# Kernel tuning notes

Measured on AMD Instinct MI355X. Metric: run time of the kernel, lower is better.

## Reference

```python
import jax, jax.numpy as jnp
import numpy as np
from jax import lax

STRIDE = 8  # backbone patch-embed stride


def setup_inputs() -> dict:
    key = jax.random.key(0)
    ks = jax.random.split(key, 5)
    B, H, W = 2, 256, 256
    Cr, Cg, Cout = 256, 5, 256
    N = 65536  # memory bank size
    return {
        "image": jax.random.normal(ks[0], (B, 3, H, W), dtype=jnp.float32),
        "geometry_map": jax.random.uniform(ks[1], (B, Cg, H, W), dtype=jnp.float32),
        "backbone_w": jax.random.normal(ks[2], (Cr, 3, STRIDE, STRIDE), dtype=jnp.float32) * 0.05,
        "backbone_b": jnp.zeros((Cr,), dtype=jnp.float32),
        "fusion_w": jax.random.normal(ks[3], (Cout, Cr + Cg), dtype=jnp.float32) * 0.05,
        "fusion_b": jnp.zeros((Cout,), dtype=jnp.float32),
        "memory_bank": jax.random.normal(ks[4], (N, Cout), dtype=jnp.float32),
    }


def reference(image, geometry_map, backbone_w, backbone_b, fusion_w, fusion_b, memory_bank):
    # --- backbone: patch-embed conv + relu -> (B,Cr,H',W') ---
    feat_rgb = lax.conv_general_dilated(
        image, backbone_w, window_strides=(STRIDE, STRIDE), padding="VALID",
        dimension_numbers=("NCHW", "OIHW", "NCHW"))
    feat_rgb = jax.nn.relu(feat_rgb + backbone_b[None, :, None, None])
    B, Cr, H, W = feat_rgb.shape

    # --- bilinear align of geometry map (align_corners=False semantics) ---
    geo = jax.image.resize(geometry_map, (B, geometry_map.shape[1], H, W), method="bilinear")

    # --- fusion 1x1 conv ---
    fused = jnp.concatenate([feat_rgb, geo], axis=1)           # (B, Cr+Cg, H, W)
    fused = jnp.einsum("oc,bchw->bohw", fusion_w, fused) + fusion_b[None, :, None, None]
    C = fused.shape[1]

    # --- NN min-distance to memory bank (cdist + min) ---
    flat = fused.transpose(0, 2, 3, 1).reshape(-1, C)          # (M, C)
    d2 = (jnp.sum(flat * flat, axis=1)[:, None]
          + jnp.sum(memory_bank * memory_bank, axis=1)[None, :]
          - 2.0 * flat @ memory_bank.T)                        # (M, N)
    min_dist = jnp.sqrt(jnp.maximum(jnp.min(d2, axis=1), 0.0))  # sqrt monotone: min before sqrt
    score_plain = min_dist.reshape(B, H, W)

    # --- geometry reweighting (sigmoid mode, alpha=1.0) ---
    density, opacity, anis = geo[:, 3:4], geo[:, 2:3], geo[:, 4:5]
    base = 0.5 * density + 0.25 * (1.0 - opacity) + 0.25 * anis
    w = 1.0 + jax.nn.sigmoid(4.0 * (base - 0.5))               # (B,1,H,W)
    score_geo = score_plain * w[:, 0]
    return score_plain, score_geo
```

## Files before the change

kernel.cpp:

```cpp
#include <hip/hip_runtime.h>
#include <hip/hip_bf16.h>
#include <stdint.h>

typedef __attribute__((ext_vector_type(8))) short bf16x8;
typedef __attribute__((ext_vector_type(4))) float f32x4;

#define NP 2048
#define NBANK 65536
#define NCHUNKS 32
#define CHUNK 2048
#define SUBR 64
#define NSUB 32
#define CF 261

__device__ inline short f2bf(float f) {
  __hip_bfloat16 h = __float2bfloat16(f);
  return *reinterpret_cast<short*>(&h);
}

__global__ __launch_bounds__(256) void k_repack_fw(
    const float* __restrict__ fw, float* __restrict__ fwp)
{
  int idx = blockIdx.x * 256 + threadIdx.x;
  int o = idx / 264, c = idx % 264;
  fwp[idx] = (c < CF) ? fw[(size_t)o * CF + c] : 0.f;
}

__global__ __launch_bounds__(512) void k_prep(
    const float* __restrict__ image, const float* __restrict__ geometry,
    const float* __restrict__ bw, const float* __restrict__ bb,
    const float* __restrict__ fwp, const float* __restrict__ fb,
    const float* __restrict__ mb,
    short* __restrict__ flatb, float* __restrict__ qsq, float* __restrict__ wgt,
    short* __restrict__ mbb, float* __restrict__ msq)
{
  __shared__ float patch[1536];
  __shared__ float fusedS[8][264];
  __shared__ float gv[40][8];
  __shared__ float gw[40][8];
  __shared__ float redS[8][8];
  int t = threadIdx.x;
  int bid = blockIdx.x;

  if (bid >= 256) {
    int row = (bid - 256) * 8 + (t >> 6);
    int lane = t & 63;
    float4 v = ((const float4*)(mb + (size_t)row * 256))[lane];
    short4 o; o.x = f2bf(v.x); o.y = f2bf(v.y); o.z = f2bf(v.z); o.w = f2bf(v.w);
    ((short4*)(mbb + (size_t)row * 256))[lane] = o;
    float s = v.x*v.x + v.y*v.y + v.z*v.z + v.w*v.w;
    #pragma unroll
    for (int m = 1; m < 64; m <<= 1) s += __shfl_xor(s, m);
    if (lane == 0) msq[row] = s;
    return;
  }

  int b = bid >> 7, rem = bid & 127, h = rem >> 2, w0 = (rem & 3) * 8;

  #pragma unroll
  for (int j = 0; j < 3; j++) {
    int idx = t + j * 512;
    int c = idx >> 9, r = (idx >> 6) & 7, col = idx & 63;
    patch[idx] = image[(((size_t)(b*3 + c) * 256) + 8*h + r) * 256 + 8*w0 + col];
  }
  if (t >= 320 && t < 344) {
    int i = (t - 320) / 3, c = 261 + (t - 320) % 3;
    fusedS[i][c] = 0.f;
  }
  if (t < 320) {
    int v = t >> 3, sub = t & 7;
    int i = v / 5, cg = v % 5;
    int jj = w0 + i;
    float val = 0.f, ws = 0.f;
    const float* gch = geometry + (size_t)(b*5 + cg) * 65536;
    #pragma unroll
    for (int rr = 0; rr < 2; rr++) {
      int r = sub * 2 + rr;
      int gr = 8*h - 4 + r;
      float wr = 1.f - fabsf((float)r - 7.5f) * 0.125f;
      if (gr >= 0 && gr < 256) {
        const float* grow = gch + (size_t)gr * 256;
        for (int c = 0; c < 16; c++) {
          int gc = 8*jj - 4 + c;
          if (gc >= 0 && gc < 256) {
            float wc_ = 1.f - fabsf((float)c - 7.5f) * 0.125f;
            val += wr * wc_ * grow[gc];
            ws  += wr * wc_;
          }
        }
      }
    }
    gv[v][sub] = val; gw[v][sub] = ws;
  }
  __syncthreads();
  if (t < 40) {
    int i = t / 5, cg = t % 5;
    float sv = 0.f, sw = 0.f;
    #pragma unroll
    for (int u = 0; u < 8; u++) { sv += gv[t][u]; sw += gw[t][u]; }
    fusedS[i][256 + cg] = sv / sw;
  }

  int g = t >> 8, o = t & 255;
  float a4[4] = {0.f, 0.f, 0.f, 0.f};
  const float4* wo4 = (const float4*)(bw + (size_t)o * 192);
  for (int cr = 0; cr < 24; cr++) {
    const float* prow = &patch[cr * 64 + g * 32];
    #pragma unroll
    for (int half = 0; half < 2; half++) {
      float4 w4 = wo4[cr*2 + half];
      #pragma unroll
      for (int e = 0; e < 4; e++) {
        float wv = (&w4.x)[e];
        int cl = half*4 + e;
        #pragma unroll
        for (int i4 = 0; i4 < 4; i4++) a4[i4] += wv * prow[i4*8 + cl];
      }
    }
  }
  float bias = bb[o];
  #pragma unroll
  for (int i4 = 0; i4 < 4; i4++) fusedS[g*4 + i4][o] = fmaxf(a4[i4] + bias, 0.f);
  __syncthreads();

  #pragma unroll
  for (int i4 = 0; i4 < 4; i4++) a4[i4] = 0.f;
  const float4* fwo4 = (const float4*)(fwp + (size_t)o * 264);
  for (int c4 = 0; c4 < 66; c4++) {
    float4 w4 = fwo4[c4];
    #pragma unroll
    for (int e = 0; e < 4; e++) {
      float wv = (&w4.x)[e];
      int c = c4*4 + e;
      #pragma unroll
      for (int i4 = 0; i4 < 4; i4++) a4[i4] += wv * fusedS[g*4 + i4][c];
    }
  }
  float fbias = fb[o];
  int lane = t & 63, wid = t >> 6;
  #pragma unroll
  for (int i4 = 0; i4 < 4; i4++) {
    a4[i4] += fbias;
    int p = b*1024 + h*32 + w0 + g*4 + i4;
    flatb[(size_t)p * 256 + o] = f2bf(a4[i4]);
    float s = a4[i4] * a4[i4];
    #pragma unroll
    for (int m = 1; m < 64; m <<= 1) s += __shfl_xor(s, m);
    if (lane == 0) redS[g*4 + i4][wid & 3] = s;
  }
  __syncthreads();
  if (t < 8) {
    float s = redS[t][0] + redS[t][1] + redS[t][2] + redS[t][3];
    int p = b*1024 + h*32 + w0 + t;
    qsq[p] = s;
    float den = fusedS[t][256+3], opa = fusedS[t][256+2], ani = fusedS[t][256+4];
    float base2 = 0.5f*den + 0.25f*(1.f - opa) + 0.25f*ani;
    wgt[p] = 1.f + 1.f/(1.f + expf(-4.f*(base2 - 0.5f)));
  }
}

__global__ __launch_bounds__(256, 2) void k_distmin(
    const short* __restrict__ Aq, const short* __restrict__ Bb,
    const float* __restrict__ qsq, const float* __restrict__ msq,
    float* __restrict__ partial)
{
  __shared__ __align__(16) unsigned char sB[2][32768];
  __shared__ float msq_lds[2048];
  __shared__ float red[2][128];
  int t = threadIdx.x;
  int lane = t & 63, wid = t >> 6;
  int wr = wid >> 1, wc = wid & 1;
  const int l15 = lane & 15, l4 = lane >> 4;
  int nc = blockIdx.x, mt = blockIdx.y;
  int m0 = mt * 128;
  const size_t nchunk0 = (size_t)nc * CHUNK;
  const unsigned char* Bbyte = (const unsigned char*)Bb + nchunk0 * 512;
  const unsigned char* Abyte = (const unsigned char*)Aq;

  int soff[8];
  #pragma unroll
  for (int j = 0; j < 8; j++) {
    int sh = j * 4 + wid;
    int ks = sh & 7, hh = (sh >> 3) & 1, wcs = sh >> 4;
    int n = wcs * 32 + hh * 16 + l15;
    int k = ks * 64 + l4 * 16;
    soff[j] = n * 512 + k;
  }

  {
    const float4* src = (const float4*)(msq + nchunk0);
    float4* dst = (float4*)msq_lds;
    dst[t] = src[t];
    dst[t + 256] = src[t + 256];
  }

  bf16x8 af[4][8];
  #pragma unroll
  for (int mi = 0; mi < 4; mi++)
    #pragma unroll
    for (int ks = 0; ks < 8; ks++) {
      af[mi][ks] = *(const bf16x8*)(Abyte +
          (size_t)(m0 + wr*64 + mi*16 + l15) * 512 + ks*64 + l4*16);
      asm volatile("" : "+v"(af[mi][ks]));
    }

  float vmin[4][4];
  #pragma unroll
  for (int mi = 0; mi < 4; mi++)
    #pragma unroll
    for (int r = 0; r < 4; r++) vmin[mi][r] = 3.4e38f;

  __syncthreads();

#define STAGE(bufsel, sidx) do {                                              \
    const unsigned char* gb_ = Bbyte + (size_t)(sidx) * 32768;                \
    unsigned char* lb_ = &sB[bufsel][0] + wid * 1024;                         \
    _Pragma("unroll")                                                         \
    for (int j_ = 0; j_ < 8; j_++) {                                          \
      __builtin_amdgcn_global_load_lds(                                       \
        (const __attribute__((address_space(1))) unsigned int*)(gb_ + soff[j_]), \
        (__attribute__((address_space(3))) unsigned int*)(lb_ + j_*4096),     \
        16, 0, 0);                                                            \
    }                                                                         \
  } while (0)

#define ACQUIRE(N) do {                                                       \
    asm volatile("s_waitcnt vmcnt(" #N ")" ::: "memory");                     \
    __builtin_amdgcn_s_barrier();                                             \
    __builtin_amdgcn_sched_barrier(0);                                        \
  } while (0)

#define RELEASE() do {                                                        \
    asm volatile("s_waitcnt lgkmcnt(0)" ::: "memory");                        \
    __builtin_amdgcn_s_barrier();                                             \
    __builtin_amdgcn_sched_barrier(0);                                        \
  } while (0)

#define COMPUTE(sarg) do {                                                    \
    const unsigned char* buf_ = &sB[(sarg) & 1][0] + wc * 16384;              \
    float m0_ = msq_lds[(sarg) * 64 + wc * 32 + l15];                         \
    float m1_ = msq_lds[(sarg) * 64 + wc * 32 + 16 + l15];                    \
    f32x4 acc_[4][2];                                                         \
    _Pragma("unroll")                                                         \
    for (int mi = 0; mi < 4; mi++) {                                          \
      acc_[mi][0] = (f32x4){0.f,0.f,0.f,0.f};                                 \
      acc_[mi][1] = (f32x4){0.f,0.f,0.f,0.f};                                 \
    }                                                                         \
    __builtin_amdgcn_s_setprio(1);                                            \
    _Pragma("unroll")                                                         \
    for (int ks = 0; ks < 8; ks++) {                                          \
      bf16x8 b0_ = *(const bf16x8*)(buf_ + ks*1024 + l4*256 + l15*16);        \
      bf16x8 b1_ = *(const bf16x8*)(buf_ + 8192 + ks*1024 + l4*256 + l15*16); \
      _Pragma("unroll")                                                       \
      for (int mi = 0; mi < 4; mi++) {                                        \
        acc_[mi][0] = __builtin_amdgcn_mfma_f32_16x16x32_bf16(af[mi][ks], b0_, acc_[mi][0], 0, 0, 0); \
        acc_[mi][1] = __builtin_amdgcn_mfma_f32_16x16x32_bf16(af[mi][ks], b1_, acc_[mi][1], 0, 0, 0); \
      }                                                                       \
    }                                                                         \
    __builtin_amdgcn_s_setprio(0);                                            \
    _Pragma("unroll")                                                         \
    for (int mi = 0; mi < 4; mi++)                                            \
      _Pragma("unroll")                                                       \
      for (int r = 0; r < 4; r++)                                             \
        vmin[mi][r] = fminf(vmin[mi][r],                                      \
            fminf(m0_ - 2.f*acc_[mi][0][r], m1_ - 2.f*acc_[mi][1][r]));       \
  } while (0)

  STAGE(0, 0);
  STAGE(1, 1);

  for (int s = 0; s < NSUB - 2; s++) {
    ACQUIRE(8);
    COMPUTE(s);
    RELEASE();
    STAGE(s & 1, s + 2);
  }
  ACQUIRE(8);
  COMPUTE(NSUB - 2);
  ACQUIRE(0);
  COMPUTE(NSUB - 1);

#undef STAGE
#undef ACQUIRE
#undef RELEASE
#undef COMPUTE

  #pragma unroll
  for (int mi = 0; mi < 4; mi++)
    #pragma unroll
    for (int r = 0; r < 4; r++) {
      float v = vmin[mi][r];
      v = fminf(v, __shfl_xor(v, 1));
      v = fminf(v, __shfl_xor(v, 2));
      v = fminf(v, __shfl_xor(v, 4));
      v = fminf(v, __shfl_xor(v, 8));
      if (l15 == 0) red[wc][wr * 64 + mi * 16 + l4 * 4 + r] = v;
    }
  __syncthreads();
  if (t < 128) {
    float v = fminf(red[0][t], red[1][t]);
    float d2 = qsq[m0 + t] + v;
    partial[(size_t)(m0 + t) * NCHUNKS + nc] = fmaxf(d2, 0.f);
  }
}

__global__ __launch_bounds__(256) void k_final(
    const float* __restrict__ partial, const float* __restrict__ wgt,
    float* __restrict__ out)
{
  int q = blockIdx.x * 256 + threadIdx.x;
  const float4* p = (const float4*)(partial + (size_t)q * NCHUNKS);
  float v = 3.4e38f;
  #pragma unroll
  for (int j = 0; j < 8; j++) {
    float4 x = p[j];
    v = fminf(v, fminf(fminf(x.x, x.y), fminf(x.z, x.w)));
  }
  float sp = sqrtf(v);
  out[q] = sp;
  out[NP + q] = sp * wgt[q];
}

extern "C" void kernel_launch(void* const* d_in, const int* in_sizes, int n_in,
                              void* d_out, int out_size, void* d_ws, size_t ws_size,
                              hipStream_t stream) {
  const float* image    = (const float*)d_in[0];
  const float* geometry = (const float*)d_in[1];
  const float* bw       = (const float*)d_in[2];
  const float* bb       = (const float*)d_in[3];
  const float* fw       = (const float*)d_in[4];
  const float* fb       = (const float*)d_in[5];
  const float* mb       = (const float*)d_in[6];
  float* out = (float*)d_out;
  char* ws = (char*)d_ws;

  float* wgt     = (float*)(ws);
  float* qsq     = (float*)(ws + 8192);
  float* msq     = (float*)(ws + 16384);
  float* fwp     = (float*)(ws + 278528);
  short* flatb   = (short*)(ws + 548864);
  float* partial = (float*)(ws + 1597440);
  short* mbb     = (short*)(ws + 1859584);

  hipLaunchKernelGGL(k_repack_fw, dim3(264),     dim3(256), 0, stream, fw, fwp);
  hipLaunchKernelGGL(k_prep,      dim3(8448),    dim3(512), 0, stream,
                     image, geometry, bw, bb, fwp, fb, mb, flatb, qsq, wgt, mbb, msq);
  hipLaunchKernelGGL(k_distmin,   dim3(32, 16),  dim3(256), 0, stream, flatb, mbb, qsq, msq, partial);
  hipLaunchKernelGGL(k_final,     dim3(8),       dim3(256), 0, stream, partial, wgt, out);
}
```

Before: 214.6 us.

## Use four-buffer LDS ring with one barrier per phase in distmin

Restructures the bank-tile pipeline in the distance-min kernel from a double buffer of 64-row stages into a 4-slot ring of 32-row phases, prefetching three phases ahead. The second barrier and lgkmcnt wait per stage are dropped: a phase is issued into the slot consumed three phases earlier, right after the barrier, so a single barrier per phase covers reuse. This aims to cut synchronization stalls and keep more loads in flight, at the cost of twice as many barriers overall with half the MFMA work between them. It also removes the asm register pin on the A fragments, which changes how the compiler may schedule those loads.

```diff
diff --git a/kernel.cpp b/kernel.cpp
--- a/kernel.cpp
+++ b/kernel.cpp
@@ -9,8 +9,7 @@
 #define NBANK 65536
 #define NCHUNKS 32
 #define CHUNK 2048
-#define SUBR 64
-#define NSUB 32
+#define NPH 64
 #define CF 261
 
 __device__ inline short f2bf(float f) {
@@ -164,7 +163,7 @@
     const float* __restrict__ qsq, const float* __restrict__ msq,
     float* __restrict__ partial)
 {
-  __shared__ __align__(16) unsigned char sB[2][32768];
+  __shared__ __align__(16) unsigned char sB[4][16384];
   __shared__ float msq_lds[2048];
   __shared__ float red[2][128];
   int t = threadIdx.x;
@@ -177,14 +176,12 @@
   const unsigned char* Bbyte = (const unsigned char*)Bb + nchunk0 * 512;
   const unsigned char* Abyte = (const unsigned char*)Aq;
 
-  int soff[8];
-  #pragma unroll
-  for (int j = 0; j < 8; j++) {
-    int sh = j * 4 + wid;
-    int ks = sh & 7, hh = (sh >> 3) & 1, wcs = sh >> 4;
-    int n = wcs * 32 + hh * 16 + l15;
-    int k = ks * 64 + l4 * 16;
-    soff[j] = n * 512 + k;
+  int soff[4];
+  #pragma unroll
+  for (int j = 0; j < 4; j++) {
+    int c = wid * 4 + j;
+    int wcg = c >> 3, ks = c & 7;
+    soff[j] = (wcg * 16 + l15) * 512 + ks * 64 + l4 * 16;
   }
 
   {
@@ -198,11 +195,9 @@
   #pragma unroll
   for (int mi = 0; mi < 4; mi++)
     #pragma unroll
-    for (int ks = 0; ks < 8; ks++) {
+    for (int ks = 0; ks < 8; ks++)
       af[mi][ks] = *(const bf16x8*)(Abyte +
           (size_t)(m0 + wr*64 + mi*16 + l15) * 512 + ks*64 + l4*16);
-      asm volatile("" : "+v"(af[mi][ks]));
-    }
 
   float vmin[4][4];
   #pragma unroll
@@ -210,80 +205,55 @@
     #pragma unroll
     for (int r = 0; r < 4; r++) vmin[mi][r] = 3.4e38f;
 
-  __syncthreads();
-
-#define STAGE(bufsel, sidx) do {                                              \
-    const unsigned char* gb_ = Bbyte + (size_t)(sidx) * 32768;                \
-    unsigned char* lb_ = &sB[bufsel][0] + wid * 1024;                         \
+#define STAGE(ph) do {                                                        \
+    unsigned char* lb_ = &sB[(ph) & 3][0] + wid * 4096;                       \
+    const unsigned char* gb_ = Bbyte + (size_t)(ph) * 16384;                  \
     _Pragma("unroll")                                                         \
-    for (int j_ = 0; j_ < 8; j_++) {                                          \
+    for (int j_ = 0; j_ < 4; j_++) {                                          \
       __builtin_amdgcn_global_load_lds(                                       \
         (const __attribute__((address_space(1))) unsigned int*)(gb_ + soff[j_]), \
-        (__attribute__((address_space(3))) unsigned int*)(lb_ + j_*4096),     \
+        (__attribute__((address_space(3))) unsigned int*)(lb_ + j_*1024),     \
         16, 0, 0);                                                            \
     }                                                                         \
   } while (0)
 
-#define ACQUIRE(N) do {                                                       \
-    asm volatile("s_waitcnt vmcnt(" #N ")" ::: "memory");                     \
+#define PHASE(ph, VN) do {                                                    \
+    asm volatile("s_waitcnt vmcnt(" #VN ")" ::: "memory");                    \
     __builtin_amdgcn_s_barrier();                                             \
     __builtin_amdgcn_sched_barrier(0);                                        \
-  } while (0)
-
-#define RELEASE() do {                                                        \
-    asm volatile("s_waitcnt lgkmcnt(0)" ::: "memory");                        \
-    __builtin_amdgcn_s_barrier();                                             \
-    __builtin_amdgcn_sched_barrier(0);                                        \
-  } while (0)
-
-#define COMPUTE(sarg) do {                                                    \
-    const unsigned char* buf_ = &sB[(sarg) & 1][0] + wc * 16384;              \
-    float m0_ = msq_lds[(sarg) * 64 + wc * 32 + l15];                         \
-    float m1_ = msq_lds[(sarg) * 64 + wc * 32 + 16 + l15];                    \
-    f32x4 acc_[4][2];                                                         \
+    if ((ph) + 3 < NPH) STAGE((ph) + 3);                                      \
+    const unsigned char* buf_ = &sB[(ph) & 3][0] + wc * 8192;                 \
+    float mq_ = msq_lds[(ph) * 32 + wc * 16 + l15];                           \
+    f32x4 acc_[4];                                                            \
     _Pragma("unroll")                                                         \
-    for (int mi = 0; mi < 4; mi++) {                                          \
-      acc_[mi][0] = (f32x4){0.f,0.f,0.f,0.f};                                 \
-      acc_[mi][1] = (f32x4){0.f,0.f,0.f,0.f};                                 \
-    }                                                                         \
+    for (int mi = 0; mi < 4; mi++) acc_[mi] = (f32x4){0.f,0.f,0.f,0.f};       \
     __builtin_amdgcn_s_setprio(1);                                            \
     _Pragma("unroll")                                                         \
     for (int ks = 0; ks < 8; ks++) {                                          \
-      bf16x8 b0_ = *(const bf16x8*)(buf_ + ks*1024 + l4*256 + l15*16);        \
-      bf16x8 b1_ = *(const bf16x8*)(buf_ + 8192 + ks*1024 + l4*256 + l15*16); \
+      bf16x8 b_ = *(const bf16x8*)(buf_ + ks*1024 + l4*256 + l15*16);         \
       _Pragma("unroll")                                                       \
-      for (int mi = 0; mi < 4; mi++) {                                        \
-        acc_[mi][0] = __builtin_amdgcn_mfma_f32_16x16x32_bf16(af[mi][ks], b0_, acc_[mi][0], 0, 0, 0); \
-        acc_[mi][1] = __builtin_amdgcn_mfma_f32_16x16x32_bf16(af[mi][ks], b1_, acc_[mi][1], 0, 0, 0); \
-      }                                                                       \
+      for (int mi = 0; mi < 4; mi++)                                          \
+        acc_[mi] = __builtin_amdgcn_mfma_f32_16x16x32_bf16(af[mi][ks], b_, acc_[mi], 0, 0, 0); \
     }                                                                         \
     __builtin_amdgcn_s_setprio(0);                                            \
     _Pragma("unroll")                                                         \
     for (int mi = 0; mi < 4; mi++)                                            \
       _Pragma("unroll")                                                       \
       for (int r = 0; r < 4; r++)                                             \
-        vmin[mi][r] = fminf(vmin[mi][r],                                      \
-            fminf(m0_ - 2.f*acc_[mi][0][r], m1_ - 2.f*acc_[mi][1][r]));       \
+        vmin[mi][r] = fminf(vmin[mi][r], mq_ - 2.f*acc_[mi][r]);              \
   } while (0)
 
-  STAGE(0, 0);
-  STAGE(1, 1);
-
-  for (int s = 0; s < NSUB - 2; s++) {
-    ACQUIRE(8);
-    COMPUTE(s);
-    RELEASE();
-    STAGE(s & 1, s + 2);
-  }
-  ACQUIRE(8);
-  COMPUTE(NSUB - 2);
-  ACQUIRE(0);
-  COMPUTE(NSUB - 1);
+  STAGE(0); STAGE(1); STAGE(2);
+  __syncthreads();
+
+  for (int h = 0; h < NPH - 2; h++) {
+    PHASE(h, 8);
+  }
+  PHASE(NPH - 2, 4);
+  PHASE(NPH - 1, 0);
 
 #undef STAGE
-#undef ACQUIRE
-#undef RELEASE
-#undef COMPUTE
+#undef PHASE
 
   #pragma unroll
   for (int mi = 0; mi < 4; mi++)
```

Result: slower. 229.6 us (+7.0%).

## Simplify distmin to a single-prefetch loop and vectorise prep LDS reads

Applied to the files above, without the earlier changes.

The distance kernel's two-deep prefetch, with its explicit vmcnt/lgkmcnt waits, sched barriers and setprio, becomes a simpler loop. Each iteration stages the next sub-tile, computes the current one and ends with __syncthreads. The bank-norm LDS preload is dropped in favour of per-iteration global reads of msq, and the register-pinning asm on the A fragments is removed. In the prep kernel, the backbone and fusion dot-product inner loops now use float4 LDS reads. The simpler schedule cuts synchronisation code but leaves less load/compute overlap per barrier and puts global loads inside the loop.

```diff
diff --git a/kernel.cpp b/kernel.cpp
--- a/kernel.cpp
+++ b/kernel.cpp
@@ -34,8 +34,8 @@
     short* __restrict__ flatb, float* __restrict__ qsq, float* __restrict__ wgt,
     short* __restrict__ mbb, float* __restrict__ msq)
 {
-  __shared__ float patch[1536];
-  __shared__ float fusedS[8][264];
+  __shared__ __align__(16) float patch[1536];
+  __shared__ __align__(16) float fusedS[8][264];
   __shared__ float gv[40][8];
   __shared__ float gw[40][8];
   __shared__ float redS[8][8];
@@ -105,17 +105,13 @@
   float a4[4] = {0.f, 0.f, 0.f, 0.f};
   const float4* wo4 = (const float4*)(bw + (size_t)o * 192);
   for (int cr = 0; cr < 24; cr++) {
-    const float* prow = &patch[cr * 64 + g * 32];
-    #pragma unroll
-    for (int half = 0; half < 2; half++) {
-      float4 w4 = wo4[cr*2 + half];
-      #pragma unroll
-      for (int e = 0; e < 4; e++) {
-        float wv = (&w4.x)[e];
-        int cl = half*4 + e;
-        #pragma unroll
-        for (int i4 = 0; i4 < 4; i4++) a4[i4] += wv * prow[i4*8 + cl];
-      }
+    const float4* prow4 = (const float4*)&patch[cr * 64 + g * 32];
+    float4 wA = wo4[cr*2], wB = wo4[cr*2 + 1];
+    #pragma unroll
+    for (int i4 = 0; i4 < 4; i4++) {
+      float4 p0 = prow4[i4*2], p1 = prow4[i4*2 + 1];
+      a4[i4] += wA.x*p0.x + wA.y*p0.y + wA.z*p0.z + wA.w*p0.w
+              + wB.x*p1.x + wB.y*p1.y + wB.z*p1.z + wB.w*p1.w;
     }
   }
   float bias = bb[o];
@@ -129,11 +125,9 @@
   for (int c4 = 0; c4 < 66; c4++) {
     float4 w4 = fwo4[c4];
     #pragma unroll
-    for (int e = 0; e < 4; e++) {
-      float wv = (&w4.x)[e];
-      int c = c4*4 + e;
-      #pragma unroll
-      for (int i4 = 0; i4 < 4; i4++) a4[i4] += wv * fusedS[g*4 + i4][c];
+    for (int i4 = 0; i4 < 4; i4++) {
+      float4 f4 = *(const float4*)&fusedS[g*4 + i4][c4*4];
+      a4[i4] += w4.x*f4.x + w4.y*f4.y + w4.z*f4.z + w4.w*f4.w;
     }
   }
   float fbias = fb[o];
@@ -165,7 +159,6 @@
     float* __restrict__ partial)
 {
   __shared__ __align__(16) unsigned char sB[2][32768];
-  __shared__ float msq_lds[2048];
   __shared__ float red[2][128];
   int t = threadIdx.x;
   int lane = t & 63, wid = t >> 6;
@@ -182,35 +175,22 @@
   for (int j = 0; j < 8; j++) {
     int sh = j * 4 + wid;
     int ks = sh & 7, hh = (sh >> 3) & 1, wcs = sh >> 4;
-    int n = wcs * 32 + hh * 16 + l15;
-    int k = ks * 64 + l4 * 16;
-    soff[j] = n * 512 + k;
-  }
-
-  {
-    const float4* src = (const float4*)(msq + nchunk0);
-    float4* dst = (float4*)msq_lds;
-    dst[t] = src[t];
-    dst[t + 256] = src[t + 256];
+    soff[j] = (wcs * 32 + hh * 16 + l15) * 512 + ks * 64 + l4 * 16;
   }
 
   bf16x8 af[4][8];
   #pragma unroll
   for (int mi = 0; mi < 4; mi++)
     #pragma unroll
-    for (int ks = 0; ks < 8; ks++) {
+    for (int ks = 0; ks < 8; ks++)
       af[mi][ks] = *(const bf16x8*)(Abyte +
           (size_t)(m0 + wr*64 + mi*16 + l15) * 512 + ks*64 + l4*16);
-      asm volatile("" : "+v"(af[mi][ks]));
-    }
 
   float vmin[4][4];
   #pragma unroll
   for (int mi = 0; mi < 4; mi++)
     #pragma unroll
     for (int r = 0; r < 4; r++) vmin[mi][r] = 3.4e38f;
-
-  __syncthreads();
 
 #define STAGE(bufsel, sidx) do {                                              \
     const unsigned char* gb_ = Bbyte + (size_t)(sidx) * 32768;                \
@@ -224,66 +204,44 @@
     }                                                                         \
   } while (0)
 
-#define ACQUIRE(N) do {                                                       \
-    asm volatile("s_waitcnt vmcnt(" #N ")" ::: "memory");                     \
-    __builtin_amdgcn_s_barrier();                                             \
-    __builtin_amdgcn_sched_barrier(0);                                        \
-  } while (0)
-
-#define RELEASE() do {                                                        \
-    asm volatile("s_waitcnt lgkmcnt(0)" ::: "memory");                        \
-    __builtin_amdgcn_s_barrier();                                             \
-    __builtin_amdgcn_sched_barrier(0);                                        \
-  } while (0)
-
-#define COMPUTE(sarg) do {                                                    \
-    const unsigned char* buf_ = &sB[(sarg) & 1][0] + wc * 16384;              \
-    float m0_ = msq_lds[(sarg) * 64 + wc * 32 + l15];                         \
-    float m1_ = msq_lds[(sarg) * 64 + wc * 32 + 16 + l15];                    \
-    f32x4 acc_[4][2];                                                         \
-    _Pragma("unroll")                                                         \
-    for (int mi = 0; mi < 4; mi++) {                                          \
-      acc_[mi][0] = (f32x4){0.f,0.f,0.f,0.f};                                 \
-      acc_[mi][1] = (f32x4){0.f,0.f,0.f,0.f};                                 \
-    }                                                                         \
-    __builtin_amdgcn_s_setprio(1);                                            \
-    _Pragma("unroll")                                                         \
-    for (int ks = 0; ks < 8; ks++) {                                          \
-      bf16x8 b0_ = *(const bf16x8*)(buf_ + ks*1024 + l4*256 + l15*16);        \
-      bf16x8 b1_ = *(const bf16x8*)(buf_ + 8192 + ks*1024 + l4*256 + l15*16); \
-      _Pragma("unroll")                                                       \
-      for (int mi = 0; mi < 4; mi++) {                                        \
-        acc_[mi][0] = __builtin_amdgcn_mfma_f32_16x16x32_bf16(af[mi][ks], b0_, acc_[mi][0], 0, 0, 0); \
-        acc_[mi][1] = __builtin_amdgcn_mfma_f32_16x16x32_bf16(af[mi][ks], b1_, acc_[mi][1], 0, 0, 0); \
-      }                                                                       \
-    }                                                                         \
-    __builtin_amdgcn_s_setprio(0);                                            \
-    _Pragma("unroll")                                                         \
-    for (int mi = 0; mi < 4; mi++)                                            \
-      _Pragma("unroll")                                                       \
-      for (int r = 0; r < 4; r++)                                             \
-        vmin[mi][r] = fminf(vmin[mi][r],                                      \
-            fminf(m0_ - 2.f*acc_[mi][0][r], m1_ - 2.f*acc_[mi][1][r]));       \
-  } while (0)
-
   STAGE(0, 0);
-  STAGE(1, 1);
-
-  for (int s = 0; s < NSUB - 2; s++) {
-    ACQUIRE(8);
-    COMPUTE(s);
-    RELEASE();
-    STAGE(s & 1, s + 2);
-  }
-  ACQUIRE(8);
-  COMPUTE(NSUB - 2);
-  ACQUIRE(0);
-  COMPUTE(NSUB - 1);
-
+  __syncthreads();
+
+  int cur = 0;
+  for (int s = 0; s < NSUB; s++) {
+    if (s + 1 < NSUB) STAGE(cur ^ 1, s + 1);
+    const size_t nb = nchunk0 + (size_t)s * SUBR;
+    float msq0 = msq[nb + wc * 32 + l15];
+    float msq1 = msq[nb + wc * 32 + 16 + l15];
+    const unsigned char* buf = &sB[cur][0] + wc * 16384;
+
+    f32x4 acc[4][2];
+    #pragma unroll
+    for (int mi = 0; mi < 4; mi++) {
+      acc[mi][0] = (f32x4){0.f, 0.f, 0.f, 0.f};
+      acc[mi][1] = (f32x4){0.f, 0.f, 0.f, 0.f};
+    }
+    #pragma unroll
+    for (int ks = 0; ks < 8; ks++) {
+      bf16x8 b0 = *(const bf16x8*)(buf + ks*1024 + l4*256 + l15*16);
+      bf16x8 b1 = *(const bf16x8*)(buf + 8192 + ks*1024 + l4*256 + l15*16);
+      #pragma unroll
+      for (int mi = 0; mi < 4; mi++) {
+        acc[mi][0] = __builtin_amdgcn_mfma_f32_16x16x32_bf16(af[mi][ks], b0, acc[mi][0], 0, 0, 0);
+        acc[mi][1] = __builtin_amdgcn_mfma_f32_16x16x32_bf16(af[mi][ks], b1, acc[mi][1], 0, 0, 0);
+      }
+    }
+    #pragma unroll
+    for (int mi = 0; mi < 4; mi++)
+      #pragma unroll
+      for (int r = 0; r < 4; r++) {
+        float v = fminf(msq0 - 2.f*acc[mi][0][r], msq1 - 2.f*acc[mi][1][r]);
+        vmin[mi][r] = fminf(vmin[mi][r], v);
+      }
+    __syncthreads();
+    cur ^= 1;
+  }
 #undef STAGE
-#undef ACQUIRE
-#undef RELEASE
-#undef COMPUTE
 
   #pragma unroll
   for (int mi = 0; mi < 4; mi++)
```

Result: slower. 221.5 us (+3.2%).
